# Kernel optimization log

Hardware: AMD Instinct MI355X
Metric: run time of the kernel (lower is better)

## Reference

```python
import jax, jax.numpy as jnp
import numpy as np

D_MODEL = 1024
N_HEADS = 16
D_K = D_MODEL // N_HEADS  # 64
D_FF = 2688
THETA = 10000.0
EPS = 1e-5
B, S = 2, 2048


def _rmsnorm(x, w):
    xf = x.astype(jnp.float32)
    ms = jnp.mean(xf * xf, axis=-1, keepdims=True)
    return (xf * w * jax.lax.rsqrt(ms + EPS)).astype(x.dtype)


def _rope(x, cos, sin):
    # x: [B, S, H, D_K]; cos/sin: [S, D_K//2]
    xe = x[..., 0::2]
    xo = x[..., 1::2]
    c = cos[None, :, None, :]
    s = sin[None, :, None, :]
    re = xe * c - xo * s
    ro = xe * s + xo * c
    # interleave back to even/odd layout
    return jnp.stack([re, ro], axis=-1).reshape(x.shape)


def setup_inputs() -> dict:
    key = jax.random.key(0)
    ks = jax.random.split(key, 12)
    sc = 0.02  # keep activations numerically sane (stand-in for trunc_normal init)
    return {
        "x": jax.random.normal(ks[0], (B, S, D_MODEL), dtype=jnp.float32),
        "ln1_w": jax.random.normal(ks[1], (D_MODEL,), dtype=jnp.float32) * sc + 1.0,
        "q_w": jax.random.normal(ks[2], (D_MODEL, D_MODEL), dtype=jnp.float32) * sc,
        "k_w": jax.random.normal(ks[3], (D_MODEL, D_MODEL), dtype=jnp.float32) * sc,
        "v_w": jax.random.normal(ks[4], (D_MODEL, D_MODEL), dtype=jnp.float32) * sc,
        "o_w": jax.random.normal(ks[5], (D_MODEL, D_MODEL), dtype=jnp.float32) * sc,
        "ln2_w": jax.random.normal(ks[6], (D_MODEL,), dtype=jnp.float32) * sc + 1.0,
        "w1_w": jax.random.normal(ks[7], (D_FF, D_MODEL), dtype=jnp.float32) * sc,
        "w3_w": jax.random.normal(ks[8], (D_FF, D_MODEL), dtype=jnp.float32) * sc,
        "w2_w": jax.random.normal(ks[9], (D_MODEL, D_FF), dtype=jnp.float32) * sc,
        "token_positions": jnp.arange(S, dtype=jnp.int32),
    }


def reference(x, ln1_w, q_w, k_w, v_w, o_w, ln2_w, w1_w, w3_w, w2_w, token_positions):
    b, s, _ = x.shape
    # --- pre-norm attention sublayer ---
    h = _rmsnorm(x, ln1_w)
    Q = (h @ q_w.T).reshape(b, s, N_HEADS, D_K)
    K = (h @ k_w.T).reshape(b, s, N_HEADS, D_K)
    V = (h @ v_w.T).reshape(b, s, N_HEADS, D_K)

    # RoPE tables from token positions
    pos = token_positions.astype(jnp.float32)                      # [S]
    kk = jnp.arange(D_K // 2, dtype=jnp.float32)
    inv_freq = THETA ** (-2.0 * kk / D_K)                          # [D_K/2]
    ang = pos[:, None] * inv_freq[None, :]                          # [S, D_K/2]
    cos, sin = jnp.cos(ang), jnp.sin(ang)

    Qr = _rope(Q, cos, sin)
    Kr = _rope(K, cos, sin)

    scale = 1.0 / jnp.sqrt(jnp.float32(D_K))
    scores = jnp.einsum("bqhd,bkhd->bhqk", Qr, Kr) * scale          # [B,H,S,S]
    causal = jnp.tril(jnp.ones((s, s), dtype=bool))
    scores = jnp.where(causal[None, None], scores, jnp.float32(-10000.0))
    attn = jax.nn.softmax(scores, axis=-1)
    ctx = jnp.einsum("bhqk,bkhd->bqhd", attn, V).reshape(b, s, D_MODEL)
    x1 = x + ctx @ o_w.T

    # --- pre-norm SwiGLU FFN sublayer ---
    h2 = _rmsnorm(x1, ln2_w)
    g = h2 @ w1_w.T                                                 # [B,S,D_FF]
    u = h2 @ w3_w.T
    ffn = (g * jax.nn.sigmoid(g) * u) @ w2_w.T
    return x1 + ffn
```

## Files before the change

kernel.cpp:

```cpp
#include <hip/hip_runtime.h>
#include <cstdint>

#define DM   1024
#define NH   16
#define DK   64
#define DFF  2688
#define SEQ  2048
#define BB   2
#define MTOT (BB*SEQ)

typedef __attribute__((ext_vector_type(8))) short short8;
typedef __attribute__((ext_vector_type(4))) float f32x4;

typedef const __attribute__((address_space(1))) void* gaddr_t;
typedef __attribute__((address_space(3))) void* laddr_t;
#define GLOAD_LDS16(g, l) __builtin_amdgcn_global_load_lds((gaddr_t)(g), (laddr_t)(l), 16, 0, 0)
#define MFMA16(a, b, c) __builtin_amdgcn_mfma_f32_16x16x32_bf16((a), (b), (c), 0, 0, 0)
#define WAIT_LDS() __builtin_amdgcn_s_waitcnt(0xc07f)

__device__ __forceinline__ float bf2f(unsigned short u) {
    union { unsigned int i; float f; } v; v.i = ((unsigned int)u) << 16; return v.f;
}
__device__ __forceinline__ unsigned short f2bf(float f) {
    union { float f; unsigned int i; } v; v.f = f;
    unsigned int r = v.i + 0x7fffu + ((v.i >> 16) & 1u);
    return (unsigned short)(r >> 16);
}
__device__ __forceinline__ unsigned long long pack4bf(float a, float b, float c, float d) {
    return (unsigned long long)f2bf(a) | ((unsigned long long)f2bf(b) << 16)
         | ((unsigned long long)f2bf(c) << 32) | ((unsigned long long)f2bf(d) << 48);
}

__global__ __launch_bounds__(256)
void convert_k(const float* __restrict__ src, unsigned short* __restrict__ dst,
               int cols, int rmul, int roff, int n4) {
    const int i = blockIdx.x * 256 + threadIdx.x;
    if (i >= n4) return;
    const int e = i * 4;
    const int r = e / cols, c = e - r * cols;
    const float4 v = *(const float4*)(src + e);
    ushort4 o;
    o.x = f2bf(v.x); o.y = f2bf(v.y); o.z = f2bf(v.z); o.w = f2bf(v.w);
    *(ushort4*)(dst + (size_t)(r * rmul + roff) * cols + c) = o;
}

__global__ __launch_bounds__(256)
void rmsnorm_k(const float* __restrict__ x, const float* __restrict__ w,
               unsigned short* __restrict__ out) {
    const int row = blockIdx.x;
    const int tid = threadIdx.x;
    const float4 v = ((const float4*)(x + (size_t)row * DM))[tid];
    float ss = v.x * v.x + v.y * v.y + v.z * v.z + v.w * v.w;
#pragma unroll
    for (int off = 32; off > 0; off >>= 1) ss += __shfl_down(ss, off, 64);
    __shared__ float sred[4];
    const int wave = tid >> 6, lane = tid & 63;
    if (lane == 0) sred[wave] = ss;
    __syncthreads();
    const float tot = sred[0] + sred[1] + sred[2] + sred[3];
    const float rinv = rsqrtf(tot * (1.0f / DM) + 1e-5f);
    const float4 wv = ((const float4*)w)[tid];
    ushort4 o;
    o.x = f2bf(v.x * wv.x * rinv);
    o.y = f2bf(v.y * wv.y * rinv);
    o.z = f2bf(v.z * wv.z * rinv);
    o.w = f2bf(v.w * wv.w * rinv);
    ((ushort4*)(out + (size_t)row * DM))[tid] = o;
}

template <int EPI>
__global__ __launch_bounds__(256)
void gemm_bt(const unsigned short* __restrict__ A,
             const unsigned short* __restrict__ B,
             unsigned short* __restrict__ Cb,
             float* __restrict__ Cf,
             const float* __restrict__ R,
             int N, int K) {
    __shared__ unsigned short As[4096];
    __shared__ unsigned short Bs[4096];
    const int tid = threadIdx.x;
    const int wave = tid >> 6, lane = tid & 63;
    const int l15 = lane & 15, quad = lane >> 4;
    const int m0 = blockIdx.y * 128, n0 = blockIdx.x * 128;
    const int wr = (wave >> 1) * 64, wc = (wave & 1) * 64;

    const f32x4 z4 = {0.f, 0.f, 0.f, 0.f};
    f32x4 acc[4][4];
#pragma unroll
    for (int i = 0; i < 4; i++)
#pragma unroll
        for (int j = 0; j < 4; j++) acc[i][j] = z4;

    const int c0 = tid, c1 = 256 + tid;
    const int k80 = c0 >> 7, mm0 = c0 & 127;
    const int k81 = c1 >> 7, mm1 = c1 & 127;
    const unsigned short* a0 = A + (size_t)(m0 + mm0) * K + k80 * 8;
    const unsigned short* a1 = A + (size_t)(m0 + mm1) * K + k81 * 8;
    const unsigned short* b0 = B + (size_t)(n0 + mm0) * K + k80 * 8;
    const unsigned short* b1 = B + (size_t)(n0 + mm1) * K + k81 * 8;
    unsigned short* lA0 = As + (wave * 64) * 8;
    unsigned short* lA1 = As + (256 + wave * 64) * 8;
    unsigned short* lB0 = Bs + (wave * 64) * 8;
    unsigned short* lB1 = Bs + (256 + wave * 64) * 8;

    for (int k0 = 0; k0 < K; k0 += 32) {
        __syncthreads();
        GLOAD_LDS16(a0 + k0, lA0);
        GLOAD_LDS16(a1 + k0, lA1);
        GLOAD_LDS16(b0 + k0, lB0);
        GLOAD_LDS16(b1 + k0, lB1);
        __syncthreads();
        short8 af[4], bg[4];
#pragma unroll
        for (int t = 0; t < 4; t++)
            af[t] = *(const short8*)(As + (quad * 128 + wr + t * 16 + l15) * 8);
#pragma unroll
        for (int t = 0; t < 4; t++)
            bg[t] = *(const short8*)(Bs + (quad * 128 + wc + t * 16 + l15) * 8);
#pragma unroll
        for (int i = 0; i < 4; i++)
#pragma unroll
            for (int j = 0; j < 4; j++)
                acc[i][j] = MFMA16(af[i], bg[j], acc[i][j]);
    }

#pragma unroll
    for (int i = 0; i < 4; i++) {
        const int r = m0 + wr + i * 16 + quad * 4;
#pragma unroll
        for (int j = 0; j < 4; j++) {
            const int cc = n0 + wc + j * 16 + l15;
#pragma unroll
            for (int reg = 0; reg < 4; reg++) {
                const size_t idx = (size_t)(r + reg) * N + cc;
                if (EPI == 0) Cb[idx] = f2bf(acc[i][j][reg]);
                else          Cf[idx] = acc[i][j][reg] + R[idx];
            }
        }
    }
}

__global__ void rope_tab_k(const int* __restrict__ pos, float* __restrict__ tab) {
    const int s = blockIdx.x, t = threadIdx.x;
    const int kk = t & 31;
    const float ang = (float)pos[s] * __expf(-0.28782313662f * (float)kk);
    tab[s * 64 + t] = (t < 32) ? cosf(ang) : sinf(ang);
}

__global__ __launch_bounds__(256)
void rope_k(const unsigned short* __restrict__ qkv, const float* __restrict__ tab,
            unsigned short* __restrict__ Qr, unsigned short* __restrict__ Kr) {
    const int m = blockIdx.x;
    const int s = m & (SEQ - 1), b = m >> 11;
    const int tid = threadIdx.x;
#pragma unroll
    for (int i = 0; i < 2; i++) {
        const int pr = i * 256 + tid;
        const int h = pr >> 5, k = pr & 31;
        const float cs = tab[s * 64 + k];
        const float sn = tab[s * 64 + 32 + k];
        const size_t so = (size_t)m * 3072 + h * 64 + 2 * k;
        const size_t doff = ((size_t)(b * NH + h) * SEQ + s) * DK + 2 * k;
        const unsigned int q2 = *(const unsigned int*)(qkv + so);
        float xe = bf2f((unsigned short)(q2 & 0xffffu));
        float xo = bf2f((unsigned short)(q2 >> 16));
        *(unsigned int*)(Qr + doff) =
            (unsigned int)f2bf(xe * cs - xo * sn) | ((unsigned int)f2bf(xe * sn + xo * cs) << 16);
        const unsigned int k2 = *(const unsigned int*)(qkv + so + 1024);
        xe = bf2f((unsigned short)(k2 & 0xffffu));
        xo = bf2f((unsigned short)(k2 >> 16));
        *(unsigned int*)(Kr + doff) =
            (unsigned int)f2bf(xe * cs - xo * sn) | ((unsigned int)f2bf(xe * sn + xo * cs) << 16);
    }
}

__global__ __launch_bounds__(256)
void vtrans_k(const unsigned short* __restrict__ qkv, unsigned short* __restrict__ Vt) {
    __shared__ unsigned short tile[64 * 72];
    const int bh = blockIdx.y;
    const int b = bh >> 4, h = bh & 15;
    const int s0 = blockIdx.x * 64;
    const int tid = threadIdx.x;
#pragma unroll
    for (int i = 0; i < 2; i++) {
        const int idx = i * 256 + tid;
        const int sl = idx >> 3, d8 = (idx & 7) * 8;
        const uint4 v = *(const uint4*)(qkv + (size_t)(b * SEQ + s0 + sl) * 3072 + 2048 + h * 64 + d8);
        *(uint4*)(tile + sl * 72 + d8) = v;
    }
    __syncthreads();
#pragma unroll
    for (int i = 0; i < 2; i++) {
        const int idx = i * 256 + tid;
        const int d = idx >> 3, s8 = (idx & 7) * 8;
        unsigned short tmp[8] __attribute__((aligned(16)));
#pragma unroll
        for (int j = 0; j < 8; j++) tmp[j] = tile[(s8 + j) * 72 + d];
        *(uint4*)(Vt + ((size_t)bh * DK + d) * SEQ + s0 + s8) = *(const uint4*)tmp;
    }
}

template <bool MASK>
__device__ __forceinline__ void softmax_tile(f32x4 st[4], float& li, unsigned short* Pw,
                                             int l15, int quad, int j0, int myq) {
    float lsum = 0.f;
#pragma unroll
    for (int t = 0; t < 4; t++) {
#pragma unroll
        for (int r = 0; r < 4; r++) {
            float v = st[t][r] * 0.125f;
            if (MASK) {
                const int key = j0 + t * 16 + quad * 4 + r;
                if (key > myq) v = -1e30f;
            }
            const float p = __expf(v);
            st[t][r] = p;
            lsum += p;
        }
        *(unsigned long long*)(Pw + l15 * 72 + t * 16 + quad * 4) =
            pack4bf(st[t][0], st[t][1], st[t][2], st[t][3]);
    }
    li += lsum;
}

__global__ __launch_bounds__(256, 2)
void attn_k(const unsigned short* __restrict__ Qr, const unsigned short* __restrict__ Kr,
            const unsigned short* __restrict__ Vt, unsigned short* __restrict__ ctx) {
    __shared__ unsigned short KVl[2][8192];
    __shared__ unsigned short Pl[4 * 2 * 1152];
    const int tid = threadIdx.x;
    const int wave = tid >> 6, lane = tid & 63;
    const int l15 = lane & 15, quad = lane >> 4;
    const int bh = blockIdx.y, b = bh >> 4, h = bh & 15;
    const int g = blockIdx.x;
    const int qtA = g * 4 + wave, qtB = 127 - qtA;
    const int q0A = qtA * 16, q0B = qtB * 16;
    const int countA = g + 1, countB = 32 - g;
    const unsigned short* Kb = Kr + (size_t)bh * SEQ * DK;
    const unsigned short* Vb = Vt + (size_t)bh * DK * SEQ;

    const unsigned short* QbA = Qr + ((size_t)bh * SEQ + q0A) * DK;
    const unsigned short* QbB = Qr + ((size_t)bh * SEQ + q0B) * DK;
    const short8 qfA0 = *(const short8*)(QbA + l15 * DK + quad * 8);
    const short8 qfA1 = *(const short8*)(QbA + l15 * DK + 32 + quad * 8);
    const short8 qfB0 = *(const short8*)(QbB + l15 * DK + quad * 8);
    const short8 qfB1 = *(const short8*)(QbB + l15 * DK + 32 + quad * 8);

    const int slot0 = wave * 128 + lane, slot1 = slot0 + 64;
    const int ck0 = slot0 >> 3, s0 = slot0 & 7;
    const int ck1 = slot1 >> 3, s1 = slot1 & 7;
    const unsigned short* kp0 = Kb + ck0 * 64 + (s0 ^ (ck0 & 7)) * 8;
    const unsigned short* kp1 = Kb + ck1 * 64 + (s1 ^ (ck1 & 7)) * 8;
    const unsigned short* vp0 = Vb + ck0 * 2048 + (s0 ^ (ck0 & 7)) * 8;
    const unsigned short* vp1 = Vb + ck1 * 2048 + (s1 ^ (ck1 & 7)) * 8;
    const int kb0 = wave * 1024, kb1 = kb0 + 512;

    unsigned short* PA = Pl + (wave * 2 + 0) * 1152;
    unsigned short* PB = Pl + (wave * 2 + 1) * 1152;

    const f32x4 z4 = {0.f, 0.f, 0.f, 0.f};
    f32x4 oA[4], oB[4];
#pragma unroll
    for (int d = 0; d < 4; d++) { oA[d] = z4; oB[d] = z4; }
    float liA = 0.f, liB = 0.f;
    const int myqA = q0A + l15, myqB = q0B + l15;
    const int xr = l15 & 7;

    GLOAD_LDS16(kp0, &KVl[0][kb0]);
    GLOAD_LDS16(kp1, &KVl[0][kb1]);
    GLOAD_LDS16(vp0, &KVl[0][4096 + kb0]);
    GLOAD_LDS16(vp1, &KVl[0][4096 + kb1]);
    kp0 += 4096; kp1 += 4096; vp0 += 64; vp1 += 64;

    for (int j = 0; j < countB; ++j) {
        const int bf = j & 1;
        const unsigned short* Kl = KVl[bf];
        const unsigned short* Vl = KVl[bf] + 4096;
        __syncthreads();
        if (j + 1 < countB) {
            GLOAD_LDS16(kp0, &KVl[bf ^ 1][kb0]);
            GLOAD_LDS16(kp1, &KVl[bf ^ 1][kb1]);
            GLOAD_LDS16(vp0, &KVl[bf ^ 1][4096 + kb0]);
            GLOAD_LDS16(vp1, &KVl[bf ^ 1][4096 + kb1]);
            kp0 += 4096; kp1 += 4096; vp0 += 64; vp1 += 64;
        }
        const int j0 = j * 64;
        short8 kf[4][2];
#pragma unroll
        for (int t = 0; t < 4; t++) {
            const unsigned short* kr = Kl + (t * 16 + l15) * 64;
            kf[t][0] = *(const short8*)(kr + (quad ^ xr) * 8);
            kf[t][1] = *(const short8*)(kr + ((4 + quad) ^ xr) * 8);
        }
        f32x4 stB[4];
#pragma unroll
        for (int t = 0; t < 4; t++)
            stB[t] = MFMA16(kf[t][1], qfB1, MFMA16(kf[t][0], qfB0, z4));
        const bool doA = (j < countA);
        if (doA) {
            f32x4 stA[4];
#pragma unroll
            for (int t = 0; t < 4; t++)
                stA[t] = MFMA16(kf[t][1], qfA1, MFMA16(kf[t][0], qfA0, z4));
            if (j == countA - 1) softmax_tile<true >(stA, liA, PA, l15, quad, j0, myqA);
            else                 softmax_tile<false>(stA, liA, PA, l15, quad, j0, myqA);
        }
        if (j == countB - 1) softmax_tile<true >(stB, liB, PB, l15, quad, j0, myqB);
        else                 softmax_tile<false>(stB, liB, PB, l15, quad, j0, myqB);
        WAIT_LDS();
        short8 vf[4][2];
#pragma unroll
        for (int dt = 0; dt < 4; dt++) {
            const unsigned short* vr = Vl + (dt * 16 + l15) * 64;
            vf[dt][0] = *(const short8*)(vr + (quad ^ xr) * 8);
            vf[dt][1] = *(const short8*)(vr + ((4 + quad) ^ xr) * 8);
        }
        {
            const short8 pfB0 = *(const short8*)(PB + l15 * 72 + quad * 8);
            const short8 pfB1 = *(const short8*)(PB + l15 * 72 + 32 + quad * 8);
#pragma unroll
            for (int dt = 0; dt < 4; dt++)
                oB[dt] = MFMA16(vf[dt][1], pfB1, MFMA16(vf[dt][0], pfB0, oB[dt]));
        }
        if (doA) {
            const short8 pfA0 = *(const short8*)(PA + l15 * 72 + quad * 8);
            const short8 pfA1 = *(const short8*)(PA + l15 * 72 + 32 + quad * 8);
#pragma unroll
            for (int dt = 0; dt < 4; dt++)
                oA[dt] = MFMA16(vf[dt][1], pfA1, MFMA16(vf[dt][0], pfA0, oA[dt]));
        }
    }
    liA += __shfl_xor(liA, 16, 64); liA += __shfl_xor(liA, 32, 64);
    liB += __shfl_xor(liB, 16, 64); liB += __shfl_xor(liB, 32, 64);
    const float invA = 1.0f / liA, invB = 1.0f / liB;
#pragma unroll
    for (int dt = 0; dt < 4; dt++) {
        *(unsigned long long*)(PA + l15 * 72 + dt * 16 + quad * 4) =
            pack4bf(oA[dt][0] * invA, oA[dt][1] * invA, oA[dt][2] * invA, oA[dt][3] * invA);
        *(unsigned long long*)(PB + l15 * 72 + dt * 16 + quad * 4) =
            pack4bf(oB[dt][0] * invB, oB[dt][1] * invB, oB[dt][2] * invB, oB[dt][3] * invB);
    }
    WAIT_LDS();
    const int row = lane >> 2, seg = (lane & 3) * 8;
#pragma unroll
    for (int p = 0; p < 2; p++) {
        const int cs = seg + p * 32;
        const uint4 va = *(const uint4*)(PA + row * 72 + cs);
        *(uint4*)(ctx + ((size_t)b * SEQ + q0A + row) * DM + h * DK + cs) = va;
        const uint4 vb = *(const uint4*)(PB + row * 72 + cs);
        *(uint4*)(ctx + ((size_t)b * SEQ + q0B + row) * DM + h * DK + cs) = vb;
    }
}

__global__ __launch_bounds__(256)
void silu_k(const unsigned short* __restrict__ gu, unsigned short* __restrict__ act, int npairs) {
    const int i = blockIdx.x * 256 + threadIdx.x;
    const int p0 = i * 4;
    if (p0 >= npairs) return;
    unsigned short in[8] __attribute__((aligned(16)));
    *(uint4*)in = *(const uint4*)(gu + (size_t)p0 * 2);
    unsigned short ov[8] __attribute__((aligned(8)));
#pragma unroll
    for (int j = 0; j < 4; j++) {
        const float g = bf2f(in[2 * j]);
        const float u = bf2f(in[2 * j + 1]);
        ov[j] = f2bf(g * u / (1.f + __expf(-g)));
    }
    *(ushort4*)(act + p0) = *(const ushort4*)ov;
}

extern "C" void kernel_launch(void* const* d_in, const int* in_sizes, int n_in,
                              void* d_out, int out_size, void* d_ws, size_t ws_size,
                              hipStream_t stream) {
    const float* x     = (const float*)d_in[0];
    const float* ln1_w = (const float*)d_in[1];
    const float* q_w   = (const float*)d_in[2];
    const float* k_w   = (const float*)d_in[3];
    const float* v_w   = (const float*)d_in[4];
    const float* o_w   = (const float*)d_in[5];
    const float* ln2_w = (const float*)d_in[6];
    const float* w1_w  = (const float*)d_in[7];
    const float* w3_w  = (const float*)d_in[8];
    const float* w2_w  = (const float*)d_in[9];
    const int*   tpos  = (const int*)d_in[10];
    float* out = (float*)d_out;
    char* ws = (char*)d_ws;

    unsigned short* Wqkv = (unsigned short*)(ws + 0);
    unsigned short* Wo   = (unsigned short*)(ws + 6291456);
    unsigned short* W13  = (unsigned short*)(ws + 8388608);
    unsigned short* W2   = (unsigned short*)(ws + 19398656);
    float*          X1   = (float*)(ws + 24903680);
    float*          ROPT = (float*)(ws + 24903680);
    char* base = ws + 41680896;
    unsigned short* H    = (unsigned short*)(base);
    unsigned short* QKV  = (unsigned short*)(base + 8388608);
    unsigned short* QR   = (unsigned short*)(base + 33554432);
    unsigned short* KR   = (unsigned short*)(base + 41943040);
    unsigned short* VT   = (unsigned short*)(base + 50331648);
    unsigned short* CTX  = (unsigned short*)(base);
    unsigned short* H2   = (unsigned short*)(base + 8388608);
    unsigned short* GU   = (unsigned short*)(base + 16777216);
    unsigned short* ACT  = (unsigned short*)(base + 60817408);

    convert_k<<<1024, 256, 0, stream>>>(q_w,  Wqkv, 1024, 1, 0,    262144);
    convert_k<<<1024, 256, 0, stream>>>(k_w,  Wqkv, 1024, 1, 1024, 262144);
    convert_k<<<1024, 256, 0, stream>>>(v_w,  Wqkv, 1024, 1, 2048, 262144);
    convert_k<<<1024, 256, 0, stream>>>(o_w,  Wo,   1024, 1, 0,    262144);
    convert_k<<<2688, 256, 0, stream>>>(w1_w, W13,  1024, 2, 0,    688128);
    convert_k<<<2688, 256, 0, stream>>>(w3_w, W13,  1024, 2, 1,    688128);
    convert_k<<<2688, 256, 0, stream>>>(w2_w, W2,   2688, 1, 0,    688128);
    rope_tab_k<<<2048, 64, 0, stream>>>(tpos, ROPT);

    rmsnorm_k<<<4096, 256, 0, stream>>>(x, ln1_w, H);
    gemm_bt<0><<<dim3(24, 32), 256, 0, stream>>>(H, Wqkv, QKV, nullptr, nullptr, 3072, 1024);
    rope_k<<<4096, 256, 0, stream>>>(QKV, ROPT, QR, KR);
    vtrans_k<<<dim3(32, 32), 256, 0, stream>>>(QKV, VT);
    attn_k<<<dim3(16, 32), 256, 0, stream>>>(QR, KR, VT, CTX);
    gemm_bt<1><<<dim3(8, 32), 256, 0, stream>>>(CTX, Wo, nullptr, X1, x, 1024, 1024);
    rmsnorm_k<<<4096, 256, 0, stream>>>(X1, ln2_w, H2);
    gemm_bt<0><<<dim3(42, 32), 256, 0, stream>>>(H2, W13, GU, nullptr, nullptr, 5376, 1024);
    silu_k<<<10752, 256, 0, stream>>>(GU, ACT, 11010048);
    gemm_bt<1><<<dim3(8, 32), 256, 0, stream>>>(ACT, W2, nullptr, out, X1, 1024, 2688);
}
```

Before: 482.3 us.

## Double-buffer GEMM LDS tiles, group tile rasterization, and vectorize epilogue stores

Uses two LDS buffers in the bf16 GEMM so the next K-slice's global-to-LDS load is issued before the MFMAs on the current slice, and drops one barrier per iteration. Remaps block IDs into groups of 8 row-tiles for better L2 reuse of the A and B panels. Swaps the MFMA operands so each lane holds four consecutive output columns, which allows packed 8-byte bf16 stores and float4 residual loads and stores. This doubles LDS use per block, which may lower occupancy. Overlap also depends on when the compiler inserts waitcnts around the barrier.

```diff
diff --git a/kernel.cpp b/kernel.cpp
--- a/kernel.cpp
+++ b/kernel.cpp
@@ -76,12 +76,21 @@
              float* __restrict__ Cf,
              const float* __restrict__ R,
              int N, int K) {
-    __shared__ unsigned short As[4096];
-    __shared__ unsigned short Bs[4096];
+    __shared__ unsigned short As[2][4096];
+    __shared__ unsigned short Bs[2][4096];
     const int tid = threadIdx.x;
     const int wave = tid >> 6, lane = tid & 63;
     const int l15 = lane & 15, quad = lane >> 4;
-    const int m0 = blockIdx.y * 128, n0 = blockIdx.x * 128;
+
+    const int gx = gridDim.x, gy = gridDim.y;
+    const int id = blockIdx.y * gx + blockIdx.x;
+    const int bpg = 8 * gx;
+    const int grp = id / bpg;
+    const int rem = id - grp * bpg;
+    const int gm = min(8, gy - grp * 8);
+    const int bm = grp * 8 + rem % gm;
+    const int bn = rem / gm;
+    const int m0 = bm * 128, n0 = bn * 128;
     const int wr = (wave >> 1) * 64, wc = (wave & 1) * 64;
 
     const f32x4 z4 = {0.f, 0.f, 0.f, 0.f};
@@ -98,43 +107,58 @@
     const unsigned short* a1 = A + (size_t)(m0 + mm1) * K + k81 * 8;
     const unsigned short* b0 = B + (size_t)(n0 + mm0) * K + k80 * 8;
     const unsigned short* b1 = B + (size_t)(n0 + mm1) * K + k81 * 8;
-    unsigned short* lA0 = As + (wave * 64) * 8;
-    unsigned short* lA1 = As + (256 + wave * 64) * 8;
-    unsigned short* lB0 = Bs + (wave * 64) * 8;
-    unsigned short* lB1 = Bs + (256 + wave * 64) * 8;
-
-    for (int k0 = 0; k0 < K; k0 += 32) {
+    const int lA0 = (wave * 64) * 8;
+    const int lA1 = (256 + wave * 64) * 8;
+
+    const int nk = K >> 5;
+    GLOAD_LDS16(a0, &As[0][lA0]);
+    GLOAD_LDS16(a1, &As[0][lA1]);
+    GLOAD_LDS16(b0, &Bs[0][lA0]);
+    GLOAD_LDS16(b1, &Bs[0][lA1]);
+    a0 += 32; a1 += 32; b0 += 32; b1 += 32;
+
+    for (int j = 0; j < nk; j++) {
+        const int bf = j & 1;
         __syncthreads();
-        GLOAD_LDS16(a0 + k0, lA0);
-        GLOAD_LDS16(a1 + k0, lA1);
-        GLOAD_LDS16(b0 + k0, lB0);
-        GLOAD_LDS16(b1 + k0, lB1);
-        __syncthreads();
+        if (j + 1 < nk) {
+            GLOAD_LDS16(a0, &As[bf ^ 1][lA0]);
+            GLOAD_LDS16(a1, &As[bf ^ 1][lA1]);
+            GLOAD_LDS16(b0, &Bs[bf ^ 1][lA0]);
+            GLOAD_LDS16(b1, &Bs[bf ^ 1][lA1]);
+            a0 += 32; a1 += 32; b0 += 32; b1 += 32;
+        }
         short8 af[4], bg[4];
 #pragma unroll
         for (int t = 0; t < 4; t++)
-            af[t] = *(const short8*)(As + (quad * 128 + wr + t * 16 + l15) * 8);
+            af[t] = *(const short8*)(&As[bf][(quad * 128 + wr + t * 16 + l15) * 8]);
 #pragma unroll
         for (int t = 0; t < 4; t++)
-            bg[t] = *(const short8*)(Bs + (quad * 128 + wc + t * 16 + l15) * 8);
+            bg[t] = *(const short8*)(&Bs[bf][(quad * 128 + wc + t * 16 + l15) * 8]);
 #pragma unroll
         for (int i = 0; i < 4; i++)
 #pragma unroll
-            for (int j = 0; j < 4; j++)
-                acc[i][j] = MFMA16(af[i], bg[j], acc[i][j]);
+            for (int j2 = 0; j2 < 4; j2++)
+                acc[i][j2] = MFMA16(bg[j2], af[i], acc[i][j2]);
     }
 
 #pragma unroll
     for (int i = 0; i < 4; i++) {
-        const int r = m0 + wr + i * 16 + quad * 4;
-#pragma unroll
-        for (int j = 0; j < 4; j++) {
-            const int cc = n0 + wc + j * 16 + l15;
-#pragma unroll
-            for (int reg = 0; reg < 4; reg++) {
-                const size_t idx = (size_t)(r + reg) * N + cc;
-                if (EPI == 0) Cb[idx] = f2bf(acc[i][j][reg]);
-                else          Cf[idx] = acc[i][j][reg] + R[idx];
+        const int r = m0 + wr + i * 16 + l15;
+#pragma unroll
+        for (int j2 = 0; j2 < 4; j2++) {
+            const int cc = n0 + wc + j2 * 16 + quad * 4;
+            const size_t idx = (size_t)r * N + cc;
+            if (EPI == 0) {
+                *(unsigned long long*)(Cb + idx) =
+                    pack4bf(acc[i][j2][0], acc[i][j2][1], acc[i][j2][2], acc[i][j2][3]);
+            } else {
+                const float4 rv = *(const float4*)(R + idx);
+                float4 ov;
+                ov.x = acc[i][j2][0] + rv.x;
+                ov.y = acc[i][j2][1] + rv.y;
+                ov.z = acc[i][j2][2] + rv.z;
+                ov.w = acc[i][j2][3] + rv.w;
+                *(float4*)(Cf + idx) = ov;
             }
         }
     }
```

Result: no change. 487.1 us (+1.0%).

## Deepen GEMM K-step, add narrow tiles, vectorize epilogue, fuse weight conversion

Applied to the files above, without the earlier changes.

The GEMM now loads a 64-wide K chunk per barrier pair instead of 32, which halves the number of synchronisation points per tile. It also adds a 128x64 tile variant so the two N=1024 projections launch twice as many blocks. MFMA operands are swapped so each lane holds four consecutive output columns, letting the epilogue write packed 8-byte bf16 stores or float4 residual adds instead of scalar stores. The seven weight-conversion launches are merged into one kernel that picks its source by block index. The costs are more LDS per block (which may lower occupancy) and smaller tiles that reuse data less.

```diff
diff --git a/kernel.cpp b/kernel.cpp
--- a/kernel.cpp
+++ b/kernel.cpp
@@ -32,10 +32,29 @@
 }
 
 __global__ __launch_bounds__(256)
-void convert_k(const float* __restrict__ src, unsigned short* __restrict__ dst,
-               int cols, int rmul, int roff, int n4) {
-    const int i = blockIdx.x * 256 + threadIdx.x;
-    if (i >= n4) return;
+void prep_k(const float* __restrict__ q_w, const float* __restrict__ k_w,
+            const float* __restrict__ v_w, const float* __restrict__ o_w,
+            const float* __restrict__ w1_w, const float* __restrict__ w3_w,
+            const float* __restrict__ w2_w,
+            unsigned short* __restrict__ Wqkv, unsigned short* __restrict__ Wo,
+            unsigned short* __restrict__ W13, unsigned short* __restrict__ W2) {
+    const int blk = blockIdx.x;
+    const float* src; unsigned short* dst; int cols, rmul, roff, i;
+    if (blk < 4096) {
+        const int rr = blk >> 10;
+        i = (blk & 1023) * 256 + threadIdx.x;
+        cols = 1024; rmul = 1;
+        if (rr == 0)      { src = q_w; dst = Wqkv; roff = 0; }
+        else if (rr == 1) { src = k_w; dst = Wqkv; roff = 1024; }
+        else if (rr == 2) { src = v_w; dst = Wqkv; roff = 2048; }
+        else              { src = o_w; dst = Wo;   roff = 0; }
+    } else if (blk < 6784) {
+        i = (blk - 4096) * 256 + threadIdx.x; src = w1_w; dst = W13; cols = 1024; rmul = 2; roff = 0;
+    } else if (blk < 9472) {
+        i = (blk - 6784) * 256 + threadIdx.x; src = w3_w; dst = W13; cols = 1024; rmul = 2; roff = 1;
+    } else {
+        i = (blk - 9472) * 256 + threadIdx.x; src = w2_w; dst = W2;  cols = 2688; rmul = 1; roff = 0;
+    }
     const int e = i * 4;
     const int r = e / cols, c = e - r * cols;
     const float4 v = *(const float4*)(src + e);
@@ -68,7 +87,7 @@
     ((ushort4*)(out + (size_t)row * DM))[tid] = o;
 }
 
-template <int EPI>
+template <int EPI, int TN>
 __global__ __launch_bounds__(256)
 void gemm_bt(const unsigned short* __restrict__ A,
              const unsigned short* __restrict__ B,
@@ -76,65 +95,86 @@
              float* __restrict__ Cf,
              const float* __restrict__ R,
              int N, int K) {
-    __shared__ unsigned short As[4096];
-    __shared__ unsigned short Bs[4096];
+    constexpr int NJ  = (TN == 128) ? 4 : 2;
+    constexpr int BPT = (TN == 128) ? 4 : 2;
+    __shared__ unsigned short As[8192];
+    __shared__ unsigned short Bs[TN * 64];
     const int tid = threadIdx.x;
     const int wave = tid >> 6, lane = tid & 63;
     const int l15 = lane & 15, quad = lane >> 4;
-    const int m0 = blockIdx.y * 128, n0 = blockIdx.x * 128;
-    const int wr = (wave >> 1) * 64, wc = (wave & 1) * 64;
+    const int m0 = blockIdx.y * 128, n0 = blockIdx.x * TN;
+    const int wr = (TN == 128) ? (wave >> 1) * 64 : (wave & 1) * 64;
+    const int wc = (TN == 128) ? (wave & 1) * 64 : (wave >> 1) * 32;
 
     const f32x4 z4 = {0.f, 0.f, 0.f, 0.f};
-    f32x4 acc[4][4];
+    f32x4 acc[4][NJ];
 #pragma unroll
     for (int i = 0; i < 4; i++)
 #pragma unroll
-        for (int j = 0; j < 4; j++) acc[i][j] = z4;
-
-    const int c0 = tid, c1 = 256 + tid;
-    const int k80 = c0 >> 7, mm0 = c0 & 127;
-    const int k81 = c1 >> 7, mm1 = c1 & 127;
-    const unsigned short* a0 = A + (size_t)(m0 + mm0) * K + k80 * 8;
-    const unsigned short* a1 = A + (size_t)(m0 + mm1) * K + k81 * 8;
-    const unsigned short* b0 = B + (size_t)(n0 + mm0) * K + k80 * 8;
-    const unsigned short* b1 = B + (size_t)(n0 + mm1) * K + k81 * 8;
-    unsigned short* lA0 = As + (wave * 64) * 8;
-    unsigned short* lA1 = As + (256 + wave * 64) * 8;
-    unsigned short* lB0 = Bs + (wave * 64) * 8;
-    unsigned short* lB1 = Bs + (256 + wave * 64) * 8;
-
-    for (int k0 = 0; k0 < K; k0 += 32) {
+        for (int j = 0; j < NJ; j++) acc[i][j] = z4;
+
+    const unsigned short* ap[4];
+    int albase[4];
+#pragma unroll
+    for (int i = 0; i < 4; i++) {
+        const int s = i * 256 + tid;
+        ap[i] = A + (size_t)(m0 + (s & 127)) * K + (s >> 7) * 8;
+        albase[i] = (i * 256 + wave * 64) * 8;
+    }
+    const unsigned short* bp[BPT];
+    int blbase[BPT];
+#pragma unroll
+    for (int i = 0; i < BPT; i++) {
+        const int s = i * 256 + tid;
+        const int nn = (TN == 128) ? (s & 127) : (s & 63);
+        const int k8 = (TN == 128) ? (s >> 7) : (s >> 6);
+        bp[i] = B + (size_t)(n0 + nn) * K + k8 * 8;
+        blbase[i] = (i * 256 + wave * 64) * 8;
+    }
+
+    const int nk = K >> 6;
+    for (int kc = 0; kc < nk; kc++) {
         __syncthreads();
-        GLOAD_LDS16(a0 + k0, lA0);
-        GLOAD_LDS16(a1 + k0, lA1);
-        GLOAD_LDS16(b0 + k0, lB0);
-        GLOAD_LDS16(b1 + k0, lB1);
+#pragma unroll
+        for (int i = 0; i < 4; i++) { GLOAD_LDS16(ap[i], &As[albase[i]]); ap[i] += 64; }
+#pragma unroll
+        for (int i = 0; i < BPT; i++) { GLOAD_LDS16(bp[i], &Bs[blbase[i]]); bp[i] += 64; }
         __syncthreads();
-        short8 af[4], bg[4];
-#pragma unroll
-        for (int t = 0; t < 4; t++)
-            af[t] = *(const short8*)(As + (quad * 128 + wr + t * 16 + l15) * 8);
-#pragma unroll
-        for (int t = 0; t < 4; t++)
-            bg[t] = *(const short8*)(Bs + (quad * 128 + wc + t * 16 + l15) * 8);
-#pragma unroll
-        for (int i = 0; i < 4; i++)
-#pragma unroll
-            for (int j = 0; j < 4; j++)
-                acc[i][j] = MFMA16(af[i], bg[j], acc[i][j]);
+#pragma unroll
+        for (int h = 0; h < 2; h++) {
+            short8 af[4], bg[NJ];
+#pragma unroll
+            for (int t = 0; t < 4; t++)
+                af[t] = *(const short8*)(&As[((quad + 4 * h) * 128 + wr + t * 16 + l15) * 8]);
+#pragma unroll
+            for (int t = 0; t < NJ; t++)
+                bg[t] = *(const short8*)(&Bs[((quad + 4 * h) * TN + wc + t * 16 + l15) * 8]);
+#pragma unroll
+            for (int i = 0; i < 4; i++)
+#pragma unroll
+                for (int j = 0; j < NJ; j++)
+                    acc[i][j] = MFMA16(bg[j], af[i], acc[i][j]);
+        }
     }
 
 #pragma unroll
     for (int i = 0; i < 4; i++) {
-        const int r = m0 + wr + i * 16 + quad * 4;
-#pragma unroll
-        for (int j = 0; j < 4; j++) {
-            const int cc = n0 + wc + j * 16 + l15;
-#pragma unroll
-            for (int reg = 0; reg < 4; reg++) {
-                const size_t idx = (size_t)(r + reg) * N + cc;
-                if (EPI == 0) Cb[idx] = f2bf(acc[i][j][reg]);
-                else          Cf[idx] = acc[i][j][reg] + R[idx];
+        const int r = m0 + wr + i * 16 + l15;
+#pragma unroll
+        for (int j = 0; j < NJ; j++) {
+            const int cc = n0 + wc + j * 16 + quad * 4;
+            const size_t idx = (size_t)r * N + cc;
+            if (EPI == 0) {
+                *(unsigned long long*)(Cb + idx) =
+                    pack4bf(acc[i][j][0], acc[i][j][1], acc[i][j][2], acc[i][j][3]);
+            } else {
+                const float4 rv = *(const float4*)(R + idx);
+                float4 ov;
+                ov.x = acc[i][j][0] + rv.x;
+                ov.y = acc[i][j][1] + rv.y;
+                ov.z = acc[i][j][2] + rv.z;
+                ov.w = acc[i][j][3] + rv.w;
+                *(float4*)(Cf + idx) = ov;
             }
         }
     }
@@ -403,23 +443,18 @@
     unsigned short* GU   = (unsigned short*)(base + 16777216);
     unsigned short* ACT  = (unsigned short*)(base + 60817408);
 
-    convert_k<<<1024, 256, 0, stream>>>(q_w,  Wqkv, 1024, 1, 0,    262144);
-    convert_k<<<1024, 256, 0, stream>>>(k_w,  Wqkv, 1024, 1, 1024, 262144);
-    convert_k<<<1024, 256, 0, stream>>>(v_w,  Wqkv, 1024, 1, 2048, 262144);
-    convert_k<<<1024, 256, 0, stream>>>(o_w,  Wo,   1024, 1, 0,    262144);
-    convert_k<<<2688, 256, 0, stream>>>(w1_w, W13,  1024, 2, 0,    688128);
-    convert_k<<<2688, 256, 0, stream>>>(w3_w, W13,  1024, 2, 1,    688128);
-    convert_k<<<2688, 256, 0, stream>>>(w2_w, W2,   2688, 1, 0,    688128);
+    prep_k<<<12160, 256, 0, stream>>>(q_w, k_w, v_w, o_w, w1_w, w3_w, w2_w,
+                                      Wqkv, Wo, W13, W2);
     rope_tab_k<<<2048, 64, 0, stream>>>(tpos, ROPT);
 
     rmsnorm_k<<<4096, 256, 0, stream>>>(x, ln1_w, H);
-    gemm_bt<0><<<dim3(24, 32), 256, 0, stream>>>(H, Wqkv, QKV, nullptr, nullptr, 3072, 1024);
+    gemm_bt<0,128><<<dim3(24, 32), 256, 0, stream>>>(H, Wqkv, QKV, nullptr, nullptr, 3072, 1024);
     rope_k<<<4096, 256, 0, stream>>>(QKV, ROPT, QR, KR);
     vtrans_k<<<dim3(32, 32), 256, 0, stream>>>(QKV, VT);
     attn_k<<<dim3(16, 32), 256, 0, stream>>>(QR, KR, VT, CTX);
-    gemm_bt<1><<<dim3(8, 32), 256, 0, stream>>>(CTX, Wo, nullptr, X1, x, 1024, 1024);
+    gemm_bt<1,64><<<dim3(16, 32), 256, 0, stream>>>(CTX, Wo, nullptr, X1, x, 1024, 1024);
     rmsnorm_k<<<4096, 256, 0, stream>>>(X1, ln2_w, H2);
-    gemm_bt<0><<<dim3(42, 32), 256, 0, stream>>>(H2, W13, GU, nullptr, nullptr, 5376, 1024);
+    gemm_bt<0,128><<<dim3(42, 32), 256, 0, stream>>>(H2, W13, GU, nullptr, nullptr, 5376, 1024);
     silu_k<<<10752, 256, 0, stream>>>(GU, ACT, 11010048);
-    gemm_bt<1><<<dim3(8, 32), 256, 0, stream>>>(ACT, W2, nullptr, out, X1, 1024, 2688);
-}
+    gemm_bt<1,64><<<dim3(16, 32), 256, 0, stream>>>(ACT, W2, nullptr, out, X1, 1024, 2688);
+}
```

New measurement: 457.5 us. -5.1%, faster.
